# Kernel tuning notes

Hardware: AMD Instinct MI355X
Metric: run time of the kernel (lower is better)

Reference implementation:

```python
import jax, jax.numpy as jnp
import numpy as np

N, L, E, H = 4, 4096, 1024, 1024


def setup_inputs() -> dict:
    key = jax.random.key(0)
    ks = jax.random.split(key, 7)
    s_in = 1.0 / np.sqrt(E)
    return {
        "X_embed": jax.random.normal(ks[0], (N, L, E), dtype=jnp.float32),
        "Wq": jax.random.normal(ks[1], (H, E), dtype=jnp.float32) * s_in,
        "bq": jnp.zeros((H,), dtype=jnp.float32),
        "Wk": jax.random.normal(ks[2], (H, E), dtype=jnp.float32) * s_in,
        "bk": jnp.zeros((H,), dtype=jnp.float32),
        "Wv": jax.random.normal(ks[3], (H, E), dtype=jnp.float32) * s_in,
        "bv": jnp.zeros((H,), dtype=jnp.float32),
    }


def reference(X_embed, Wq, bq, Wk, bk, Wv, bv):
    # Linear projections: (N, L, E) @ (E, H) + (H,) -> (N, L, H)
    Q = jnp.einsum('nle,he->nlh', X_embed, Wq) + bq
    K = jnp.einsum('nle,he->nlh', X_embed, Wk) + bk
    V = jnp.einsum('nle,he->nlh', X_embed, Wv) + bv
    # Scores (N, L, L); original scales by sqrt(Out.shape[2]) == sqrt(L)
    S = jnp.einsum('nah,nbh->nab', Q, K) / jnp.asarray(np.sqrt(float(L)), dtype=Q.dtype)
    # Original softmax is over dim=1 (the query axis 'a')
    A = jax.nn.softmax(S, axis=1)
    # 'nll,nlh->nlh': diagonal of A times V, elementwise over h
    diag = jnp.diagonal(A, axis1=1, axis2=2)  # (N, L)
    return diag[:, :, None] * V
```

## Files before the change

kernel.cpp:

```cpp
#include <hip/hip_runtime.h>
#include <hip/hip_bf16.h>
#include <stdint.h>

#define NB 4
#define LS 4096
#define ED 1024
#define HD 1024
#define MR (NB * LS)
#define SCALE_S (1.0f / 64.0f)

typedef __attribute__((ext_vector_type(8))) short bf16x8;
typedef __attribute__((ext_vector_type(8))) int   i32x8;
typedef __attribute__((ext_vector_type(4))) float f32x4;

__device__ __forceinline__ unsigned short f2bf(float f) {
    union { float f; uint32_t u; } x; x.f = f;
    uint32_t r = x.u + 0x7fffu + ((x.u >> 16) & 1u);
    return (unsigned short)(r >> 16);
}

__device__ __forceinline__ void load_lds16(const void* g, void* s) {
    __builtin_amdgcn_global_load_lds(
        (const __attribute__((address_space(1))) void*)g,
        (__attribute__((address_space(3))) void*)s, 16, 0, 0);
}

#define XCHUNKS (MR * ED / 4)
#define WCHUNKS (3 * ED * ED / 4)
__global__ void __launch_bounds__(256) cast_all_k(
    const float4* __restrict__ X, const float4* __restrict__ wq,
    const float4* __restrict__ wk, const float4* __restrict__ wv,
    ushort4* __restrict__ Xb, ushort4* __restrict__ Wall)
{
    const int i = blockIdx.x * 256 + threadIdx.x;
    if (i < XCHUNKS) {
        const float4 v = X[i];
        ushort4 o; o.x = f2bf(v.x); o.y = f2bf(v.y); o.z = f2bf(v.z); o.w = f2bf(v.w);
        Xb[i] = o;
    } else if (i < XCHUNKS + WCHUNKS) {
        const int j = i - XCHUNKS;
        const int s = j >> 18, jj = j & 0x3ffff;
        const float4 v = (s == 0 ? wq : s == 1 ? wk : wv)[jj];
        ushort4 o; o.x = f2bf(v.x); o.y = f2bf(v.y); o.z = f2bf(v.z); o.w = f2bf(v.w);
        Wall[j] = o;
    }
}

__global__ void __launch_bounds__(256, 2)
gemm_qk_fused(const unsigned short* __restrict__ A,
              const unsigned short* __restrict__ W,
              const float* __restrict__ bq, const float* __restrict__ bk,
              unsigned char* __restrict__ Qf8t, unsigned char* __restrict__ Kf8t,
              float* __restrict__ diag)
{
    __shared__ unsigned short As[128 * 32];
    __shared__ unsigned short Ws0[128 * 32];
    __shared__ unsigned short Ws1[128 * 32];

    const int t = threadIdx.x;
    const int wid = t >> 6, lane = t & 63, quad = lane >> 4, l16 = lane & 15;
    const int m0 = (wid >> 1) * 64, n0 = (wid & 1) * 64;
    const long blockM = (long)blockIdx.y * 128;
    const int blockN = blockIdx.x * 128;

    const char* a_g  = (const char*)(A + (blockM + (t >> 2)) * (size_t)ED + (size_t)((t & 3) * 8));
    const char* w0_g = (const char*)(W + ((size_t)blockN + (t >> 2)) * ED + (size_t)((t & 3) * 8));
    const char* w1_g = w0_g + (size_t)1024 * ED * 2;
    const size_t half = (size_t)64 * ED * 2;

    char* a_s0 = (char*)As  + wid * 1024;
    char* w0_s = (char*)Ws0 + wid * 1024;
    char* w1_s = (char*)Ws1 + wid * 1024;

    f32x4 acc[2][4][4] = {};

    for (int kt = 0; kt < ED; kt += 32) {
        const int kb = kt * 2;
        load_lds16(a_g  + kb,        a_s0);
        load_lds16(a_g  + kb + half, a_s0 + 4096);
        load_lds16(w0_g + kb,        w0_s);
        load_lds16(w0_g + kb + half, w0_s + 4096);
        load_lds16(w1_g + kb,        w1_s);
        load_lds16(w1_g + kb + half, w1_s + 4096);
        __syncthreads();

        bf16x8 aF[4];
        const char* AsB = (const char*)As;
#pragma unroll
        for (int mf = 0; mf < 4; mf++)
            aF[mf] = *(const bf16x8*)(AsB + ((m0 + mf * 16 + l16) * 32 + quad * 8) * 2);

#pragma unroll
        for (int p = 0; p < 2; p++) {
            const char* WsB = (const char*)(p == 0 ? Ws0 : Ws1);
            bf16x8 bF[4];
#pragma unroll
            for (int nf = 0; nf < 4; nf++)
                bF[nf] = *(const bf16x8*)(WsB + ((n0 + nf * 16 + l16) * 32 + quad * 8) * 2);
#pragma unroll
            for (int mf = 0; mf < 4; mf++)
#pragma unroll
                for (int nf = 0; nf < 4; nf++)
                    acc[p][mf][nf] = __builtin_amdgcn_mfma_f32_16x16x32_bf16(
                        bF[nf], aF[mf], acc[p][mf][nf], 0, 0, 0);
        }
        __syncthreads();
    }

    float dp[4] = {0.f, 0.f, 0.f, 0.f};
#pragma unroll
    for (int nf = 0; nf < 4; nf++) {
        const int col = blockN + n0 + nf * 16 + quad * 4;
        const float4 q4 = *(const float4*)(bq + col);
        const float4 k4 = *(const float4*)(bk + col);
#pragma unroll
        for (int mf = 0; mf < 4; mf++) {
            const size_t row = (size_t)(blockM + m0 + mf * 16 + l16);
            const float vq0 = acc[0][mf][nf][0] + q4.x, vq1 = acc[0][mf][nf][1] + q4.y;
            const float vq2 = acc[0][mf][nf][2] + q4.z, vq3 = acc[0][mf][nf][3] + q4.w;
            const float vk0 = acc[1][mf][nf][0] + k4.x, vk1 = acc[1][mf][nf][1] + k4.y;
            const float vk2 = acc[1][mf][nf][2] + k4.z, vk3 = acc[1][mf][nf][3] + k4.w;
            uint32_t uq = 0, uk = 0;
            uq = __builtin_amdgcn_cvt_pk_fp8_f32(vq0, vq1, uq, false);
            uq = __builtin_amdgcn_cvt_pk_fp8_f32(vq2, vq3, uq, true);
            uk = __builtin_amdgcn_cvt_pk_fp8_f32(vk0, vk1, uk, false);
            uk = __builtin_amdgcn_cvt_pk_fp8_f32(vk2, vk3, uk, true);
            const size_t f8 = (row >> 4) * 16384 + (size_t)(col >> 4) * 256
                            + (row & 15) * 16 + (col & 15);
            *(uint32_t*)(Qf8t + f8) = uq;
            *(uint32_t*)(Kf8t + f8) = uk;
            dp[mf] += vq0 * vk0 + vq1 * vk1 + vq2 * vk2 + vq3 * vk3;
        }
    }
#pragma unroll
    for (int mf = 0; mf < 4; mf++) {
        float d = dp[mf];
        d += __shfl_xor(d, 16);
        d += __shfl_xor(d, 32);
        if (quad == 0)
            atomicAdd(&diag[blockM + m0 + mf * 16 + l16], d);
    }
}

__global__ void __launch_bounds__(256)
gemm_v(const unsigned short* __restrict__ A,
       const unsigned short* __restrict__ Wv,
       const float* __restrict__ bv, float* __restrict__ outV)
{
    __shared__ unsigned short As[128 * 32];
    __shared__ unsigned short Bs[128 * 32];

    const int t = threadIdx.x;
    const int wid = t >> 6, lane = t & 63, quad = lane >> 4, l16 = lane & 15;
    const int m0 = (wid >> 1) * 64, n0 = (wid & 1) * 64;
    const long blockM = (long)blockIdx.y * 128;
    const int blockN = blockIdx.x * 128;

    const char* a_g = (const char*)(A  + (blockM + (t >> 2)) * (size_t)ED + (size_t)((t & 3) * 8));
    const char* b_g = (const char*)(Wv + ((size_t)blockN + (t >> 2)) * ED + (size_t)((t & 3) * 8));
    const size_t half = (size_t)64 * ED * 2;

    char* a_s0 = (char*)As + wid * 1024;
    char* b_s0 = (char*)Bs + wid * 1024;

    f32x4 acc[4][4] = {};

    for (int kt = 0; kt < ED; kt += 32) {
        const int kb = kt * 2;
        load_lds16(a_g + kb,        a_s0);
        load_lds16(a_g + kb + half, a_s0 + 4096);
        load_lds16(b_g + kb,        b_s0);
        load_lds16(b_g + kb + half, b_s0 + 4096);
        __syncthreads();

        bf16x8 aF[4], bF[4];
        const char* AsB = (const char*)As;
        const char* BsB = (const char*)Bs;
#pragma unroll
        for (int mf = 0; mf < 4; mf++)
            aF[mf] = *(const bf16x8*)(AsB + ((m0 + mf * 16 + l16) * 32 + quad * 8) * 2);
#pragma unroll
        for (int nf = 0; nf < 4; nf++)
            bF[nf] = *(const bf16x8*)(BsB + ((n0 + nf * 16 + l16) * 32 + quad * 8) * 2);
#pragma unroll
        for (int mf = 0; mf < 4; mf++)
#pragma unroll
            for (int nf = 0; nf < 4; nf++)
                acc[mf][nf] = __builtin_amdgcn_mfma_f32_16x16x32_bf16(
                    bF[nf], aF[mf], acc[mf][nf], 0, 0, 0);
        __syncthreads();
    }

#pragma unroll
    for (int mf = 0; mf < 4; mf++) {
        const size_t row = (size_t)(blockM + m0 + mf * 16 + l16);
#pragma unroll
        for (int nf = 0; nf < 4; nf++) {
            const int col = blockN + n0 + nf * 16 + quad * 4;
            const float4 b4 = *(const float4*)(bv + col);
            float4 o;
            o.x = acc[mf][nf][0] + b4.x; o.y = acc[mf][nf][1] + b4.y;
            o.z = acc[mf][nf][2] + b4.z; o.w = acc[mf][nf][3] + b4.w;
            *(float4*)(outV + row * 1024 + col) = o;
        }
    }
}

__global__ void __launch_bounds__(256)
gemm_f8_denom(const unsigned char* __restrict__ Qt,
              const unsigned char* __restrict__ Kt,
              float* __restrict__ denom)
{
    __shared__ __align__(16) unsigned char As[16384];
    __shared__ __align__(16) unsigned char Bs[16384];

    const int t = threadIdx.x;
    const int wid = t >> 6, lane = t & 63, quad = lane >> 4, l16 = lane & 15;
    const int m0 = (wid >> 1) * 64, n0 = (wid & 1) * 64;
    const size_t zoff = (size_t)blockIdx.z * LS * (size_t)HD;
    const unsigned char* A = Qt + zoff;
    const unsigned char* B = Kt + zoff;
    float* dn = denom + (size_t)blockIdx.z * LS;
    const int blockM = blockIdx.y * 128;
    const int blockN = blockIdx.x * 128;

    size_t aoff[4], boff[4];
#pragma unroll
    for (int j = 0; j < 4; j++) {
        const int iw = wid * 4 + j;
        const size_t lo = (size_t)((iw & 1) * 4 + (lane >> 4)) * 256 + (size_t)(lane & 15) * 16;
        aoff[j] = ((size_t)(blockM >> 4) + (iw >> 1)) * 16384 + lo;
        boff[j] = ((size_t)(blockN >> 4) + (iw >> 1)) * 16384 + lo;
    }

    f32x4 acc[4][4] = {};

    for (int kt = 0; kt < 8; kt++) {
        const size_t ko = (size_t)kt * 2048;
#pragma unroll
        for (int j = 0; j < 4; j++) {
            load_lds16(A + aoff[j] + ko, (char*)As + (wid * 4 + j) * 1024);
            load_lds16(B + boff[j] + ko, (char*)Bs + (wid * 4 + j) * 1024);
        }
        __syncthreads();

        i32x8 aF[4], bF[4];
#pragma unroll
        for (int mf = 0; mf < 4; mf++) {
            const int base = (((m0 >> 4) + mf) * 2048) + quad * 512 + l16 * 16;
            const int4 lo = *(const int4*)(As + base);
            const int4 hi = *(const int4*)(As + base + 256);
            aF[mf][0] = lo.x; aF[mf][1] = lo.y; aF[mf][2] = lo.z; aF[mf][3] = lo.w;
            aF[mf][4] = hi.x; aF[mf][5] = hi.y; aF[mf][6] = hi.z; aF[mf][7] = hi.w;
        }
#pragma unroll
        for (int nf = 0; nf < 4; nf++) {
            const int base = (((n0 >> 4) + nf) * 2048) + quad * 512 + l16 * 16;
            const int4 lo = *(const int4*)(Bs + base);
            const int4 hi = *(const int4*)(Bs + base + 256);
            bF[nf][0] = lo.x; bF[nf][1] = lo.y; bF[nf][2] = lo.z; bF[nf][3] = lo.w;
            bF[nf][4] = hi.x; bF[nf][5] = hi.y; bF[nf][6] = hi.z; bF[nf][7] = hi.w;
        }
#pragma unroll
        for (int mf = 0; mf < 4; mf++)
#pragma unroll
            for (int nf = 0; nf < 4; nf++)
                acc[mf][nf] = __builtin_amdgcn_mfma_scale_f32_16x16x128_f8f6f4(
                    aF[mf], bF[nf], acc[mf][nf],
                    0, 0,
                    0, 0x7f7f7f7f,
                    0, 0x7f7f7f7f);
        __syncthreads();
    }

#pragma unroll
    for (int nf = 0; nf < 4; nf++) {
        float s = 0.f;
#pragma unroll
        for (int mf = 0; mf < 4; mf++)
#pragma unroll
            for (int r = 0; r < 4; r++)
                s += __expf(acc[mf][nf][r] * SCALE_S);
        s += __shfl_xor(s, 16);
        s += __shfl_xor(s, 32);
        if (quad == 0)
            atomicAdd(&dn[blockN + n0 + nf * 16 + l16], s);
    }
}

__global__ void __launch_bounds__(256) finalize_k(
    float* __restrict__ out, const float* __restrict__ diag,
    const float* __restrict__ denom)
{
    const int row = blockIdx.x;
    const float sc = __expf(diag[row] * SCALE_S) / denom[row];
    float4* p = (float4*)(out + (size_t)row * HD) + threadIdx.x;
    float4 v = *p;
    v.x *= sc; v.y *= sc; v.z *= sc; v.w *= sc;
    *p = v;
}

extern "C" void kernel_launch(void* const* d_in, const int* in_sizes, int n_in,
                              void* d_out, int out_size, void* d_ws, size_t ws_size,
                              hipStream_t stream)
{
    (void)in_sizes; (void)n_in; (void)out_size; (void)ws_size;
    const float* X  = (const float*)d_in[0];
    const float* Wq = (const float*)d_in[1];
    const float* bq = (const float*)d_in[2];
    const float* Wk = (const float*)d_in[3];
    const float* bk = (const float*)d_in[4];
    const float* Wv = (const float*)d_in[5];
    const float* bv = (const float*)d_in[6];
    float* out = (float*)d_out;

    char* p = (char*)d_ws;
    unsigned short* Xb   = (unsigned short*)p; p += (size_t)MR * ED * 2;
    unsigned short* Wall = (unsigned short*)p; p += (size_t)3072 * ED * 2;
    unsigned char*  Qf8t = (unsigned char*)p;  p += (size_t)MR * HD;
    unsigned char*  Kf8t = (unsigned char*)p;  p += (size_t)MR * HD;
    float* diag  = (float*)p; p += (size_t)MR * 4;
    float* denom = (float*)p; p += (size_t)MR * 4;

    dim3 blk(256);

    cast_all_k<<<(XCHUNKS + WCHUNKS + 255) / 256, blk, 0, stream>>>(
        (const float4*)X, (const float4*)Wq, (const float4*)Wk, (const float4*)Wv,
        (ushort4*)Xb, (ushort4*)Wall);

    hipMemsetAsync(diag, 0, 2 * MR * sizeof(float), stream);

    dim3 gqk(HD / 128, MR / 128);
    gemm_qk_fused<<<gqk, blk, 0, stream>>>(Xb, Wall, bq, bk, Qf8t, Kf8t, diag);

    gemm_v<<<gqk, blk, 0, stream>>>(Xb, Wall + (size_t)2048 * ED, bv, out);

    dim3 gden(LS / 128, LS / 128, NB);
    gemm_f8_denom<<<gden, blk, 0, stream>>>(Qf8t, Kf8t, denom);

    finalize_k<<<MR, blk, 0, stream>>>(out, diag, denom);
}
```

Measured before the change: 363.6 us.

## Rewrite fused Q/K projection GEMM as 8-wave 256x128 tile with pipelined LDS

The fused Q/K GEMM is replaced with a 512-thread kernel. Each block computes a 256x128 tile with K-step 64 and uses 128 KB of dynamic LDS as a double buffer. Global-to-LDS loads are interleaved with MFMA phases under explicit waitcnt, barriers and setprio, the LDS layout is XOR-swizzled to avoid bank conflicts, and blocks are remapped for locality. The goal is to hide memory latency and raise MFMA utilization. The cost is a hand-scheduled kernel that is fragile and assumes exact shapes, with very high LDS use limiting occupancy.

New measurement: 355.8 us. 2.2% less time.

```diff
diff --git a/kernel.cpp b/kernel.cpp
--- a/kernel.cpp
+++ b/kernel.cpp
@@ -46,80 +46,158 @@
     }
 }
 
-__global__ void __launch_bounds__(256, 2)
-gemm_qk_fused(const unsigned short* __restrict__ A,
-              const unsigned short* __restrict__ W,
-              const float* __restrict__ bq, const float* __restrict__ bk,
-              unsigned char* __restrict__ Qf8t, unsigned char* __restrict__ Kf8t,
-              float* __restrict__ diag)
-{
-    __shared__ unsigned short As[128 * 32];
-    __shared__ unsigned short Ws0[128 * 32];
-    __shared__ unsigned short Ws1[128 * 32];
-
+
+__device__ __forceinline__ void read_af(bf16x8 (&af)[4][2], const char* base,
+                                        int arow, int sw7, int quad) {
+#pragma unroll
+    for (int mf = 0; mf < 4; mf++) {
+        const char* r = base + (arow + mf * 16) * 128;
+        af[mf][0] = *(const bf16x8*)(r + ((quad * 16) ^ sw7));
+        af[mf][1] = *(const bf16x8*)(r + ((64 + quad * 16) ^ sw7));
+    }
+}
+__device__ __forceinline__ void read_wf(bf16x8 (&wf)[4], const char* base,
+                                        int wrow, int ks64, int sw7, int quad) {
+#pragma unroll
+    for (int nf = 0; nf < 4; nf++)
+        wf[nf] = *(const bf16x8*)(base + (wrow + nf * 16) * 128 + ((ks64 + quad * 16) ^ sw7));
+}
+template<int KS>
+__device__ __forceinline__ void mfma16(f32x4 (&acc)[4][4], const bf16x8 (&af)[4][2],
+                                       const bf16x8 (&wf)[4]) {
+#pragma unroll
+    for (int mf = 0; mf < 4; mf++)
+#pragma unroll
+        for (int nf = 0; nf < 4; nf++)
+            acc[mf][nf] = __builtin_amdgcn_mfma_f32_16x16x32_bf16(
+                wf[nf], af[mf][KS], acc[mf][nf], 0, 0, 0);
+}
+
+#define QK_BAR() do { asm volatile("" ::: "memory"); \
+    __builtin_amdgcn_s_barrier(); asm volatile("" ::: "memory"); } while (0)
+#define PH_MID() do { QK_BAR(); \
+    asm volatile("s_waitcnt lgkmcnt(0)" ::: "memory"); \
+    __builtin_amdgcn_sched_barrier(0); \
+    __builtin_amdgcn_s_setprio(1); } while (0)
+#define PH_END() do { __builtin_amdgcn_s_setprio(0); QK_BAR(); } while (0)
+#define PH_END_VM6() do { __builtin_amdgcn_s_setprio(0); \
+    asm volatile("s_waitcnt vmcnt(6)" ::: "memory"); QK_BAR(); } while (0)
+#define PH_END_VM0() do { __builtin_amdgcn_s_setprio(0); \
+    asm volatile("s_waitcnt vmcnt(0)" ::: "memory"); QK_BAR(); } while (0)
+
+__global__ void __launch_bounds__(512, 2)
+gemm_qk_fused8(const unsigned short* __restrict__ A,
+               const unsigned short* __restrict__ W,
+               const float* __restrict__ bq, const float* __restrict__ bk,
+               unsigned char* __restrict__ Qf8t, unsigned char* __restrict__ Kf8t,
+               float* __restrict__ diag)
+{
+    extern __shared__ char lds[];
     const int t = threadIdx.x;
-    const int wid = t >> 6, lane = t & 63, quad = lane >> 4, l16 = lane & 15;
-    const int m0 = (wid >> 1) * 64, n0 = (wid & 1) * 64;
-    const long blockM = (long)blockIdx.y * 128;
-    const int blockN = blockIdx.x * 128;
-
-    const char* a_g  = (const char*)(A + (blockM + (t >> 2)) * (size_t)ED + (size_t)((t & 3) * 8));
-    const char* w0_g = (const char*)(W + ((size_t)blockN + (t >> 2)) * ED + (size_t)((t & 3) * 8));
-    const char* w1_g = w0_g + (size_t)1024 * ED * 2;
-    const size_t half = (size_t)64 * ED * 2;
-
-    char* a_s0 = (char*)As  + wid * 1024;
-    char* w0_s = (char*)Ws0 + wid * 1024;
-    char* w1_s = (char*)Ws1 + wid * 1024;
-
-    f32x4 acc[2][4][4] = {};
-
-    for (int kt = 0; kt < ED; kt += 32) {
-        const int kb = kt * 2;
-        load_lds16(a_g  + kb,        a_s0);
-        load_lds16(a_g  + kb + half, a_s0 + 4096);
-        load_lds16(w0_g + kb,        w0_s);
-        load_lds16(w0_g + kb + half, w0_s + 4096);
-        load_lds16(w1_g + kb,        w1_s);
-        load_lds16(w1_g + kb + half, w1_s + 4096);
-        __syncthreads();
-
-        bf16x8 aF[4];
-        const char* AsB = (const char*)As;
-#pragma unroll
-        for (int mf = 0; mf < 4; mf++)
-            aF[mf] = *(const bf16x8*)(AsB + ((m0 + mf * 16 + l16) * 32 + quad * 8) * 2);
-
-#pragma unroll
-        for (int p = 0; p < 2; p++) {
-            const char* WsB = (const char*)(p == 0 ? Ws0 : Ws1);
-            bf16x8 bF[4];
-#pragma unroll
-            for (int nf = 0; nf < 4; nf++)
-                bF[nf] = *(const bf16x8*)(WsB + ((n0 + nf * 16 + l16) * 32 + quad * 8) * 2);
-#pragma unroll
-            for (int mf = 0; mf < 4; mf++)
-#pragma unroll
-                for (int nf = 0; nf < 4; nf++)
-                    acc[p][mf][nf] = __builtin_amdgcn_mfma_f32_16x16x32_bf16(
-                        bF[nf], aF[mf], acc[p][mf][nf], 0, 0, 0);
-        }
-        __syncthreads();
-    }
+    const int w = t >> 6, lane = t & 63, quad = lane >> 4, l16 = lane & 15;
+    const int wm = w >> 1, wn = w & 1;
+
+    const int swz = (blockIdx.x & 7) * 64 + (blockIdx.x >> 3);
+    const long blockM = (long)(swz >> 3) * 256;
+    const int  blockN = (swz & 7) * 128;
+
+    const long srow = (long)(w * 8 + (lane >> 3)) * 2048
+                    + (long)(((lane & 7) ^ (lane >> 3)) << 4);
+    const char* gA  = (const char*)A + blockM * 2048 + srow;
+    const char* gAh = gA + 128 * 2048;
+    const char* gWq = (const char*)W + (long)blockN * 2048 + srow;
+    const char* gWk = gWq + (long)1024 * 2048;
+    char* dst = lds + w * 1024;
+
+#define ST(G, OFF, KB) do { \
+    load_lds16((G) + (KB), dst + (OFF)); \
+    load_lds16((G) + 131072 + (KB), dst + (OFF) + 8192); } while (0)
+
+    const char* A0 = lds;          const char* A1 = lds + 65536;
+    const char* Q0 = lds + 32768;  const char* Q1 = lds + 65536 + 32768;
+    const char* K0 = lds + 49152;  const char* K1 = lds + 65536 + 49152;
+
+    const int arow = wm * 64 + l16;
+    const int wrow = wn * 64 + l16;
+    const int sw7  = (l16 & 7) << 4;
+
+    f32x4 aq[4][4] = {}; f32x4 ak[4][4] = {};
+    bf16x8 aF[4][2], wF[4];
+
+    ST(gA, 0, 0); ST(gAh, 16384, 0); ST(gWq, 32768, 0); ST(gWk, 49152, 0);
+    ST(gA, 65536, 128); ST(gAh, 65536 + 16384, 128); ST(gWq, 65536 + 32768, 128);
+    asm volatile("s_waitcnt vmcnt(6)" ::: "memory");
+    QK_BAR();
+
+#pragma unroll 1
+    for (int i = 0; i < 7; ++i) {
+        const long k1 = (2L * i + 1) * 128, k2 = (2L * i + 2) * 128, k3 = (2L * i + 3) * 128;
+        read_af(aF, A0, arow, sw7, quad);
+        read_wf(wF, Q0, wrow, 0, sw7, quad);
+        ST(gWk, 65536 + 49152, k1);
+        asm volatile("s_waitcnt lgkmcnt(8)" ::: "memory");
+        PH_MID(); mfma16<0>(aq, aF, wF); PH_END();
+        read_wf(wF, Q0, wrow, 64, sw7, quad);
+        ST(gA, 0, k2);
+        PH_MID(); mfma16<1>(aq, aF, wF); PH_END();
+        read_wf(wF, K0, wrow, 0, sw7, quad);
+        ST(gAh, 16384, k2);
+        PH_MID(); mfma16<0>(ak, aF, wF); PH_END();
+        read_wf(wF, K0, wrow, 64, sw7, quad);
+        ST(gWq, 32768, k2);
+        PH_MID(); mfma16<1>(ak, aF, wF); PH_END_VM6();
+        read_af(aF, A1, arow, sw7, quad);
+        read_wf(wF, Q1, wrow, 0, sw7, quad);
+        ST(gWk, 49152, k2);
+        asm volatile("s_waitcnt lgkmcnt(8)" ::: "memory");
+        PH_MID(); mfma16<0>(aq, aF, wF); PH_END();
+        read_wf(wF, Q1, wrow, 64, sw7, quad);
+        ST(gA, 65536, k3);
+        PH_MID(); mfma16<1>(aq, aF, wF); PH_END();
+        read_wf(wF, K1, wrow, 0, sw7, quad);
+        ST(gAh, 65536 + 16384, k3);
+        PH_MID(); mfma16<0>(ak, aF, wF); PH_END();
+        read_wf(wF, K1, wrow, 64, sw7, quad);
+        ST(gWq, 65536 + 32768, k3);
+        PH_MID(); mfma16<1>(ak, aF, wF); PH_END_VM6();
+    }
+    {
+        read_af(aF, A0, arow, sw7, quad);
+        read_wf(wF, Q0, wrow, 0, sw7, quad);
+        ST(gWk, 65536 + 49152, 15L * 128);
+        asm volatile("s_waitcnt lgkmcnt(8)" ::: "memory");
+        PH_MID(); mfma16<0>(aq, aF, wF); PH_END();
+        read_wf(wF, Q0, wrow, 64, sw7, quad);
+        PH_MID(); mfma16<1>(aq, aF, wF); PH_END();
+        read_wf(wF, K0, wrow, 0, sw7, quad);
+        PH_MID(); mfma16<0>(ak, aF, wF); PH_END();
+        read_wf(wF, K0, wrow, 64, sw7, quad);
+        PH_MID(); mfma16<1>(ak, aF, wF); PH_END_VM0();
+        read_af(aF, A1, arow, sw7, quad);
+        read_wf(wF, Q1, wrow, 0, sw7, quad);
+        PH_MID(); mfma16<0>(aq, aF, wF); PH_END();
+        read_wf(wF, Q1, wrow, 64, sw7, quad);
+        PH_MID(); mfma16<1>(aq, aF, wF); PH_END();
+        read_wf(wF, K1, wrow, 0, sw7, quad);
+        PH_MID(); mfma16<0>(ak, aF, wF); PH_END();
+        read_wf(wF, K1, wrow, 64, sw7, quad);
+        PH_MID(); mfma16<1>(ak, aF, wF); PH_END();
+    }
+#undef ST
 
     float dp[4] = {0.f, 0.f, 0.f, 0.f};
 #pragma unroll
     for (int nf = 0; nf < 4; nf++) {
-        const int col = blockN + n0 + nf * 16 + quad * 4;
+        const int col = blockN + wn * 64 + nf * 16 + quad * 4;
         const float4 q4 = *(const float4*)(bq + col);
         const float4 k4 = *(const float4*)(bk + col);
 #pragma unroll
         for (int mf = 0; mf < 4; mf++) {
-            const size_t row = (size_t)(blockM + m0 + mf * 16 + l16);
-            const float vq0 = acc[0][mf][nf][0] + q4.x, vq1 = acc[0][mf][nf][1] + q4.y;
-            const float vq2 = acc[0][mf][nf][2] + q4.z, vq3 = acc[0][mf][nf][3] + q4.w;
-            const float vk0 = acc[1][mf][nf][0] + k4.x, vk1 = acc[1][mf][nf][1] + k4.y;
-            const float vk2 = acc[1][mf][nf][2] + k4.z, vk3 = acc[1][mf][nf][3] + k4.w;
+            const size_t row = (size_t)(blockM + wm * 64 + mf * 16 + l16);
+            const float vq0 = aq[mf][nf][0] + q4.x, vq1 = aq[mf][nf][1] + q4.y;
+            const float vq2 = aq[mf][nf][2] + q4.z, vq3 = aq[mf][nf][3] + q4.w;
+            const float vk0 = ak[mf][nf][0] + k4.x, vk1 = ak[mf][nf][1] + k4.y;
+            const float vk2 = ak[mf][nf][2] + k4.z, vk3 = ak[mf][nf][3] + k4.w;
             uint32_t uq = 0, uk = 0;
             uq = __builtin_amdgcn_cvt_pk_fp8_f32(vq0, vq1, uq, false);
             uq = __builtin_amdgcn_cvt_pk_fp8_f32(vq2, vq3, uq, true);
@@ -138,7 +216,7 @@
         d += __shfl_xor(d, 16);
         d += __shfl_xor(d, 32);
         if (quad == 0)
-            atomicAdd(&diag[blockM + m0 + mf * 16 + l16], d);
+            atomicAdd(&diag[blockM + wm * 64 + mf * 16 + l16], d);
     }
 }
 
@@ -324,16 +402,24 @@
 
     dim3 blk(256);
 
+    static int qk8_init = 0;
+    if (!qk8_init) {
+        hipFuncSetAttribute((const void*)gemm_qk_fused8,
+                            hipFuncAttributeMaxDynamicSharedMemorySize, 131072);
+        qk8_init = 1;
+    }
+
     cast_all_k<<<(XCHUNKS + WCHUNKS + 255) / 256, blk, 0, stream>>>(
         (const float4*)X, (const float4*)Wq, (const float4*)Wk, (const float4*)Wv,
         (ushort4*)Xb, (ushort4*)Wall);
 
     hipMemsetAsync(diag, 0, 2 * MR * sizeof(float), stream);
 
-    dim3 gqk(HD / 128, MR / 128);
-    gemm_qk_fused<<<gqk, blk, 0, stream>>>(Xb, Wall, bq, bk, Qf8t, Kf8t, diag);
-
-    gemm_v<<<gqk, blk, 0, stream>>>(Xb, Wall + (size_t)2048 * ED, bv, out);
+    gemm_qk_fused8<<<dim3(512), dim3(512), 131072, stream>>>(
+        Xb, Wall, bq, bk, Qf8t, Kf8t, diag);
+
+    dim3 gv(HD / 128, MR / 128);
+    gemm_v<<<gv, blk, 0, stream>>>(Xb, Wall + (size_t)2048 * ED, bv, out);
 
     dim3 gden(LS / 128, LS / 128, NB);
     gemm_f8_denom<<<gden, blk, 0, stream>>>(Qf8t, Kf8t, denom);
```
